# Kernel tuning notes

Measured on AMD Instinct MI355X. Metric: run time of the kernel, lower is better.

The kernel has to match this reference:

```python
import jax, jax.numpy as jnp
import numpy as np

IN_FEATURES = 2048
OUT_FEATURES = 4096
NUM_SHIFTS = 10  # perms


def setup_inputs() -> dict:
    key = jax.random.key(0)
    kx, kw = jax.random.split(key)
    x = jax.random.normal(kx, (4, 2048, IN_FEATURES), dtype=jnp.float32)
    # nn.Linear weight: (out_features, in_features), Kaiming-uniform-ish init
    bound = 1.0 / np.sqrt(IN_FEATURES)
    W = jax.random.uniform(kw, (OUT_FEATURES, IN_FEATURES), dtype=jnp.float32,
                           minval=-bound, maxval=bound)
    return {"x": x, "W": W}


def _combined_weight(W):
    # Wt: (in, out). Sum of all weight variants; sum_i(x @ W_i) == x @ sum_i(W_i).
    Wt = W.T
    Weff = Wt + jnp.flip(Wt, axis=0) + jnp.flip(Wt, axis=1)
    for i in range(NUM_SHIFTS // 2):
        Weff = Weff + jnp.roll(Wt, shift=i + 1, axis=1)
        Weff = Weff + jnp.roll(Wt, shift=i + 1, axis=0)
    return Weff  # (in, out)


def reference(x, W):
    # reg_out (x @ W.T) + flipped + rolled variants, collapsed into one GEMM
    Weff = _combined_weight(W)
    return jnp.einsum('bsi,io->bso', x, Weff)
```

## Files before the change

kernel.cpp:

```cpp
#include <hip/hip_runtime.h>
#include <hip/hip_bf16.h>
#include <stdint.h>

#define M_DIM 8192
#define K_DIM 2048
#define N_DIM 4096
#define BM 256
#define BN 256
#define BK 64
#define NT (K_DIM / BK)
#define NITER (NT / 2)

typedef __attribute__((ext_vector_type(8))) short bf16x8;
typedef __attribute__((ext_vector_type(4))) float f32x4;

__device__ __forceinline__ unsigned short f2bfu(float f) {
    __hip_bfloat16 h = __float2bfloat16(f);
    return __builtin_bit_cast(unsigned short, h);
}

__global__ __launch_bounds__(256) void prep_fused(const float* __restrict__ x,
                                                  const float* __restrict__ W,
                                                  unsigned short* __restrict__ xb,
                                                  unsigned short* __restrict__ wt) {
    const int bid = blockIdx.x;
    if (bid < N_DIM / 2) {
        __shared__ float row0[K_DIM];
        __shared__ float row1[K_DIM];
        const int o0 = bid * 2;
        const float* w0 = W + (size_t)o0 * K_DIM;
        const float* w1 = W + (size_t)(o0 + 1) * K_DIM;
#pragma unroll
        for (int t = 0; t < 2; ++t) {
            ((float4*)row0)[threadIdx.x + 256 * t] = ((const float4*)w0)[threadIdx.x + 256 * t];
            ((float4*)row1)[threadIdx.x + 256 * t] = ((const float4*)w1)[threadIdx.x + 256 * t];
        }
        __syncthreads();

        const float* rF0 = W + (size_t)(N_DIM - 1 - o0) * K_DIM;
        const float* rF1 = W + (size_t)(N_DIM - 2 - o0) * K_DIM;
        const float* rm1 = W + (size_t)((o0 - 1) & (N_DIM - 1)) * K_DIM;
        const float* rm2 = W + (size_t)((o0 - 2) & (N_DIM - 1)) * K_DIM;
        const float* rm3 = W + (size_t)((o0 - 3) & (N_DIM - 1)) * K_DIM;
        const float* rm4 = W + (size_t)((o0 - 4) & (N_DIM - 1)) * K_DIM;
        const float* rm5 = W + (size_t)((o0 - 5) & (N_DIM - 1)) * K_DIM;
        unsigned short* wo0 = wt + (size_t)o0 * K_DIM;
        unsigned short* wo1 = wo0 + K_DIM;

#pragma unroll
        for (int t = 0; t < 2; ++t) {
            const int i0 = (threadIdx.x + 256 * t) * 4;
            const float4 vF0 = *(const float4*)(rF0 + i0);
            const float4 vF1 = *(const float4*)(rF1 + i0);
            const float4 v1  = *(const float4*)(rm1 + i0);
            const float4 v2  = *(const float4*)(rm2 + i0);
            const float4 v3  = *(const float4*)(rm3 + i0);
            const float4 v4  = *(const float4*)(rm4 + i0);
            const float4 v5  = *(const float4*)(rm5 + i0);
            ushort4 ov0, ov1;
#pragma unroll
            for (int j = 0; j < 4; ++j) {
                const int i = i0 + j;
                float s0 = row0[i] + row0[K_DIM - 1 - i]
                         + row0[(i - 1) & (K_DIM - 1)] + row0[(i - 2) & (K_DIM - 1)]
                         + row0[(i - 3) & (K_DIM - 1)] + row0[(i - 4) & (K_DIM - 1)]
                         + row0[(i - 5) & (K_DIM - 1)];
                s0 += (&vF0.x)[j] + (&v1.x)[j] + (&v2.x)[j]
                    + (&v3.x)[j] + (&v4.x)[j] + (&v5.x)[j];
                (&ov0.x)[j] = f2bfu(s0);

                float s1 = row1[i] + row1[K_DIM - 1 - i]
                         + row1[(i - 1) & (K_DIM - 1)] + row1[(i - 2) & (K_DIM - 1)]
                         + row1[(i - 3) & (K_DIM - 1)] + row1[(i - 4) & (K_DIM - 1)]
                         + row1[(i - 5) & (K_DIM - 1)];
                s1 += (&vF1.x)[j] + row0[i] + (&v1.x)[j] + (&v2.x)[j]
                    + (&v3.x)[j] + (&v4.x)[j];
                (&ov1.x)[j] = f2bfu(s1);
            }
            *(ushort4*)(wo0 + i0) = ov0;
            *(ushort4*)(wo1 + i0) = ov1;
        }
    } else {
        const int idx = (bid - N_DIM / 2) * 256 + threadIdx.x;
        float4 v = ((const float4*)x)[idx];
        ushort4 o;
        o.x = f2bfu(v.x); o.y = f2bfu(v.y); o.z = f2bfu(v.z); o.w = f2bfu(v.w);
        ((ushort4*)xb)[idx] = o;
    }
}

__global__ __launch_bounds__(512, 2) void gemm8p(const unsigned short* __restrict__ Ab,
                                                 const unsigned short* __restrict__ Bt,
                                                 float* __restrict__ C) {
    __shared__ __align__(16) char smem[2 * 65536];

    const int tid  = threadIdx.x;
    const int wave = tid >> 6;
    const int lane = tid & 63;

    const int nwg = gridDim.x;
    const int cpx = nwg >> 3;
    const int wg  = (blockIdx.x & 7) * cpx + (blockIdx.x >> 3);
    const int nbn = N_DIM / BN;
    const int bm0 = (wg / nbn) * BM;
    const int bn0 = (wg % nbn) * BN;

    const int wr = wave >> 2;
    const int wc = wave & 3;

    const int srow = tid >> 3;
    const int lsw  = (lane & 7) ^ ((lane >> 3) & 7);
    const unsigned short* gA0 = Ab + (size_t)(bm0 + srow) * K_DIM + lsw * 8;
    const unsigned short* gB0 = Bt + (size_t)(bn0 + srow) * K_DIM + lsw * 8;

    const int r16  = lane & 15;
    const int x7   = lane & 7;
    const int ksl0 = (((lane >> 4)    ) ^ x7) * 16;
    const int ksl1 = (((lane >> 4) | 4) ^ x7) * 16;
    const int aRow = (wr * 128 + r16) * 128;
    const int bRow = (wc * 64  + r16) * 128 + 32768;

    f32x4  acc[8][4] = {};
    bf16x8 b[4][2];

#define STAGE_HALF(gbase, opoff, h, t, p) do {                                              \
    char* lds_ = smem + (p) * 65536 + (opoff) + (h) * 16384 + wave * 1024;                  \
    const unsigned short* g_ = (gbase) + (size_t)((h) * 128) * K_DIM + (t) * BK;            \
    __builtin_amdgcn_global_load_lds(                                                        \
        (const __attribute__((address_space(1))) unsigned int*)g_,                           \
        (__attribute__((address_space(3))) unsigned int*)lds_, 16, 0, 0);                    \
    __builtin_amdgcn_global_load_lds(                                                        \
        (const __attribute__((address_space(1))) unsigned int*)(g_ + (size_t)64 * K_DIM),    \
        (__attribute__((address_space(3))) unsigned int*)(lds_ + 8192), 16, 0, 0);           \
} while (0)

#define PHASE(P, Q, LOADB, STAGE_STMT, VM_STMT) do {                                        \
    const char* base_ = smem + (P) * 65536;                                                 \
    bf16x8 a_[2][2];                                                                        \
    if (LOADB) {                                                                            \
        _Pragma("unroll")                                                                   \
        for (int fn = 0; fn < 4; ++fn) {                                                    \
            b[fn][0] = *(const bf16x8*)(base_ + bRow + fn * 2048 + ksl0);                   \
            b[fn][1] = *(const bf16x8*)(base_ + bRow + fn * 2048 + ksl1);                   \
        }                                                                                   \
    }                                                                                       \
    a_[0][0] = *(const bf16x8*)(base_ + aRow + (Q) * 4096 + ksl0);                          \
    a_[0][1] = *(const bf16x8*)(base_ + aRow + (Q) * 4096 + ksl1);                          \
    a_[1][0] = *(const bf16x8*)(base_ + aRow + (Q) * 4096 + 2048 + ksl0);                   \
    a_[1][1] = *(const bf16x8*)(base_ + aRow + (Q) * 4096 + 2048 + ksl1);                   \
    STAGE_STMT;                                                                             \
    __builtin_amdgcn_s_barrier();                                                           \
    asm volatile("s_waitcnt lgkmcnt(0)" ::: "memory");                                      \
    __builtin_amdgcn_sched_barrier(0);                                                      \
    __builtin_amdgcn_s_setprio(1);                                                          \
    _Pragma("unroll")                                                                       \
    for (int fm = 0; fm < 2; ++fm)                                                          \
        _Pragma("unroll")                                                                   \
        for (int fn = 0; fn < 4; ++fn) {                                                    \
            acc[(Q)*2 + fm][fn] = __builtin_amdgcn_mfma_f32_16x16x32_bf16(                  \
                a_[fm][0], b[fn][0], acc[(Q)*2 + fm][fn], 0, 0, 0);                         \
            acc[(Q)*2 + fm][fn] = __builtin_amdgcn_mfma_f32_16x16x32_bf16(                  \
                a_[fm][1], b[fn][1], acc[(Q)*2 + fm][fn], 0, 0, 0);                         \
        }                                                                                   \
    __builtin_amdgcn_s_setprio(0);                                                          \
    VM_STMT;                                                                                \
    __builtin_amdgcn_s_barrier();                                                           \
} while (0)

    STAGE_HALF(gB0, 32768, 0, 0, 0);
    STAGE_HALF(gB0, 32768, 1, 0, 0);
    STAGE_HALF(gA0, 0,     0, 0, 0);
    STAGE_HALF(gA0, 0,     1, 0, 0);
    STAGE_HALF(gB0, 32768, 0, 1, 1);
    STAGE_HALF(gB0, 32768, 1, 1, 1);
    STAGE_HALF(gA0, 0,     0, 1, 1);
    asm volatile("s_waitcnt vmcnt(6)" ::: "memory");
    __builtin_amdgcn_s_barrier();

    for (int u = 0; u < NITER; ++u) {
        const bool last = (u == NITER - 1);
        const int  t1 = 2 * u + 1, t2 = 2 * u + 2, t3 = 2 * u + 3;

        PHASE(0, 0, 1, { STAGE_HALF(gA0, 0, 1, t1, 1); }, {});
        PHASE(0, 1, 0, { if (!last) STAGE_HALF(gB0, 32768, 0, t2, 0); }, {});
        PHASE(0, 2, 0, { if (!last) STAGE_HALF(gB0, 32768, 1, t2, 0); }, {});
        PHASE(0, 3, 0, { if (!last) STAGE_HALF(gA0, 0, 0, t2, 0); },
              { if (last) asm volatile("s_waitcnt vmcnt(0)" ::: "memory");
                else      asm volatile("s_waitcnt vmcnt(6)" ::: "memory"); });
        PHASE(1, 0, 1, { if (!last) STAGE_HALF(gA0, 0, 1, t2, 0); }, {});
        PHASE(1, 1, 0, { if (!last) STAGE_HALF(gB0, 32768, 0, t3, 1); }, {});
        PHASE(1, 2, 0, { if (!last) STAGE_HALF(gB0, 32768, 1, t3, 1); }, {});
        PHASE(1, 3, 0, { if (!last) STAGE_HALF(gA0, 0, 0, t3, 1); },
              { if (!last) asm volatile("s_waitcnt vmcnt(6)" ::: "memory"); });
    }
#undef PHASE
#undef STAGE_HALF

    const int crow = (lane >> 4) * 4;
    const int ccol = lane & 15;
    float* Cb = C + (size_t)(bm0 + wr * 128 + crow) * N_DIM + (bn0 + wc * 64 + ccol);
#pragma unroll
    for (int fm = 0; fm < 8; ++fm)
#pragma unroll
        for (int fn = 0; fn < 4; ++fn)
#pragma unroll
            for (int r = 0; r < 4; ++r)
                Cb[(size_t)(fm * 16 + r) * N_DIM + fn * 16] = acc[fm][fn][r];
}

extern "C" void kernel_launch(void* const* d_in, const int* in_sizes, int n_in,
                              void* d_out, int out_size, void* d_ws, size_t ws_size,
                              hipStream_t stream) {
    const float* x = (const float*)d_in[0];
    const float* W = (const float*)d_in[1];
    float* out = (float*)d_out;

    unsigned short* xb = (unsigned short*)d_ws;
    unsigned short* wt = (unsigned short*)((char*)d_ws + (size_t)M_DIM * K_DIM * 2);

    const int cvt_blocks = (M_DIM * K_DIM) / 4 / 256;
    prep_fused<<<N_DIM / 2 + cvt_blocks, 256, 0, stream>>>(x, W, xb, wt);

    dim3 grid((M_DIM / BM) * (N_DIM / BN));
    gemm8p<<<grid, 512, 0, stream>>>(xb, wt, out);
}
```

Before: 163.6 us.

## Make GEMM persistent with two tiles per workgroup and overlap epilogue with next prologue

The GEMM grid drops from 512 to 256 workgroups. Each workgroup now computes two output tiles, at M offsets 0 and 4096. The second tile's prologue global loads are issued before the first tile's C stores, so the epilogue overlaps with prefetch. The B-fragment LDS reads in the first phase are also split with staged lgkmcnt waits, letting MFMAs start before all B reads land. The cost is a fixed 256-block grid that matches the CU count, which removes tail flexibility, and the prologue writing LDS while prior reads may still be pending relies on the existing barriers.

```diff
diff --git a/kernel.cpp b/kernel.cpp
--- a/kernel.cpp
+++ b/kernel.cpp
@@ -98,20 +98,14 @@
     const int wave = tid >> 6;
     const int lane = tid & 63;
 
-    const int nwg = gridDim.x;
-    const int cpx = nwg >> 3;
-    const int wg  = (blockIdx.x & 7) * cpx + (blockIdx.x >> 3);
-    const int nbn = N_DIM / BN;
-    const int bm0 = (wg / nbn) * BM;
-    const int bn0 = (wg % nbn) * BN;
+    const int cpx = 256 >> 3;
+    const int wg  = ((int)blockIdx.x & 7) * cpx + ((int)blockIdx.x >> 3);
 
     const int wr = wave >> 2;
     const int wc = wave & 3;
 
     const int srow = tid >> 3;
     const int lsw  = (lane & 7) ^ ((lane >> 3) & 7);
-    const unsigned short* gA0 = Ab + (size_t)(bm0 + srow) * K_DIM + lsw * 8;
-    const unsigned short* gB0 = Bt + (size_t)(bn0 + srow) * K_DIM + lsw * 8;
 
     const int r16  = lane & 15;
     const int x7   = lane & 7;
@@ -119,9 +113,13 @@
     const int ksl1 = (((lane >> 4) | 4) ^ x7) * 16;
     const int aRow = (wr * 128 + r16) * 128;
     const int bRow = (wc * 64  + r16) * 128 + 32768;
-
-    f32x4  acc[8][4] = {};
+    const int crow = (lane >> 4) * 4;
+    const int ccol = lane & 15;
+
+    f32x4  acc[8][4];
     bf16x8 b[4][2];
+    const unsigned short* gA0;
+    const unsigned short* gB0;
 
 #define STAGE_HALF(gbase, opoff, h, t, p) do {                                              \
     char* lds_ = smem + (p) * 65536 + (opoff) + (h) * 16384 + wave * 1024;                  \
@@ -134,16 +132,9 @@
         (__attribute__((address_space(3))) unsigned int*)(lds_ + 8192), 16, 0, 0);           \
 } while (0)
 
-#define PHASE(P, Q, LOADB, STAGE_STMT, VM_STMT) do {                                        \
+#define PHASE(P, Q, STAGE_STMT, VM_STMT) do {                                               \
     const char* base_ = smem + (P) * 65536;                                                 \
     bf16x8 a_[2][2];                                                                        \
-    if (LOADB) {                                                                            \
-        _Pragma("unroll")                                                                   \
-        for (int fn = 0; fn < 4; ++fn) {                                                    \
-            b[fn][0] = *(const bf16x8*)(base_ + bRow + fn * 2048 + ksl0);                   \
-            b[fn][1] = *(const bf16x8*)(base_ + bRow + fn * 2048 + ksl1);                   \
-        }                                                                                   \
-    }                                                                                       \
     a_[0][0] = *(const bf16x8*)(base_ + aRow + (Q) * 4096 + ksl0);                          \
     a_[0][1] = *(const bf16x8*)(base_ + aRow + (Q) * 4096 + ksl1);                          \
     a_[1][0] = *(const bf16x8*)(base_ + aRow + (Q) * 4096 + 2048 + ksl0);                   \
@@ -167,45 +158,134 @@
     __builtin_amdgcn_s_barrier();                                                           \
 } while (0)
 
-    STAGE_HALF(gB0, 32768, 0, 0, 0);
-    STAGE_HALF(gB0, 32768, 1, 0, 0);
-    STAGE_HALF(gA0, 0,     0, 0, 0);
-    STAGE_HALF(gA0, 0,     1, 0, 0);
-    STAGE_HALF(gB0, 32768, 0, 1, 1);
-    STAGE_HALF(gB0, 32768, 1, 1, 1);
-    STAGE_HALF(gA0, 0,     0, 1, 1);
-    asm volatile("s_waitcnt vmcnt(6)" ::: "memory");
-    __builtin_amdgcn_s_barrier();
-
-    for (int u = 0; u < NITER; ++u) {
-        const bool last = (u == NITER - 1);
-        const int  t1 = 2 * u + 1, t2 = 2 * u + 2, t3 = 2 * u + 3;
-
-        PHASE(0, 0, 1, { STAGE_HALF(gA0, 0, 1, t1, 1); }, {});
-        PHASE(0, 1, 0, { if (!last) STAGE_HALF(gB0, 32768, 0, t2, 0); }, {});
-        PHASE(0, 2, 0, { if (!last) STAGE_HALF(gB0, 32768, 1, t2, 0); }, {});
-        PHASE(0, 3, 0, { if (!last) STAGE_HALF(gA0, 0, 0, t2, 0); },
-              { if (last) asm volatile("s_waitcnt vmcnt(0)" ::: "memory");
-                else      asm volatile("s_waitcnt vmcnt(6)" ::: "memory"); });
-        PHASE(1, 0, 1, { if (!last) STAGE_HALF(gA0, 0, 1, t2, 0); }, {});
-        PHASE(1, 1, 0, { if (!last) STAGE_HALF(gB0, 32768, 0, t3, 1); }, {});
-        PHASE(1, 2, 0, { if (!last) STAGE_HALF(gB0, 32768, 1, t3, 1); }, {});
-        PHASE(1, 3, 0, { if (!last) STAGE_HALF(gA0, 0, 0, t3, 1); },
-              { if (!last) asm volatile("s_waitcnt vmcnt(6)" ::: "memory"); });
-    }
+#define FN_CLUSTER(Q, FN) do {                                                              \
+    _Pragma("unroll")                                                                       \
+    for (int fm = 0; fm < 2; ++fm) {                                                        \
+        acc[(Q)*2 + fm][FN] = __builtin_amdgcn_mfma_f32_16x16x32_bf16(                      \
+            a_[fm][0], b[FN][0], acc[(Q)*2 + fm][FN], 0, 0, 0);                             \
+        acc[(Q)*2 + fm][FN] = __builtin_amdgcn_mfma_f32_16x16x32_bf16(                      \
+            a_[fm][1], b[FN][1], acc[(Q)*2 + fm][FN], 0, 0, 0);                             \
+    }                                                                                       \
+} while (0)
+
+#define PHASE_B(P, Q, STAGE_STMT, VM_STMT) do {                                             \
+    const char* base_ = smem + (P) * 65536;                                                 \
+    bf16x8 a_[2][2];                                                                        \
+    a_[0][0] = *(const bf16x8*)(base_ + aRow + (Q) * 4096 + ksl0);                          \
+    a_[0][1] = *(const bf16x8*)(base_ + aRow + (Q) * 4096 + ksl1);                          \
+    a_[1][0] = *(const bf16x8*)(base_ + aRow + (Q) * 4096 + 2048 + ksl0);                   \
+    a_[1][1] = *(const bf16x8*)(base_ + aRow + (Q) * 4096 + 2048 + ksl1);                   \
+    b[0][0] = *(const bf16x8*)(base_ + bRow + ksl0);                                        \
+    b[0][1] = *(const bf16x8*)(base_ + bRow + ksl1);                                        \
+    __builtin_amdgcn_sched_barrier(0);                                                      \
+    b[1][0] = *(const bf16x8*)(base_ + bRow + 2048 + ksl0);                                 \
+    b[1][1] = *(const bf16x8*)(base_ + bRow + 2048 + ksl1);                                 \
+    __builtin_amdgcn_sched_barrier(0);                                                      \
+    b[2][0] = *(const bf16x8*)(base_ + bRow + 4096 + ksl0);                                 \
+    b[2][1] = *(const bf16x8*)(base_ + bRow + 4096 + ksl1);                                 \
+    __builtin_amdgcn_sched_barrier(0);                                                      \
+    b[3][0] = *(const bf16x8*)(base_ + bRow + 6144 + ksl0);                                 \
+    b[3][1] = *(const bf16x8*)(base_ + bRow + 6144 + ksl1);                                 \
+    __builtin_amdgcn_sched_barrier(0);                                                      \
+    STAGE_STMT;                                                                             \
+    __builtin_amdgcn_s_barrier();                                                           \
+    asm volatile("s_waitcnt lgkmcnt(6)" ::: "memory");                                      \
+    __builtin_amdgcn_sched_barrier(0);                                                      \
+    __builtin_amdgcn_s_setprio(1);                                                          \
+    FN_CLUSTER(Q, 0);                                                                       \
+    __builtin_amdgcn_sched_barrier(0);                                                      \
+    asm volatile("s_waitcnt lgkmcnt(4)" ::: "memory");                                      \
+    __builtin_amdgcn_sched_barrier(0);                                                      \
+    FN_CLUSTER(Q, 1);                                                                       \
+    __builtin_amdgcn_sched_barrier(0);                                                      \
+    asm volatile("s_waitcnt lgkmcnt(2)" ::: "memory");                                      \
+    __builtin_amdgcn_sched_barrier(0);                                                      \
+    FN_CLUSTER(Q, 2);                                                                       \
+    __builtin_amdgcn_sched_barrier(0);                                                      \
+    asm volatile("s_waitcnt lgkmcnt(0)" ::: "memory");                                      \
+    __builtin_amdgcn_sched_barrier(0);                                                      \
+    FN_CLUSTER(Q, 3);                                                                       \
+    __builtin_amdgcn_s_setprio(0);                                                          \
+    VM_STMT;                                                                                \
+    __builtin_amdgcn_s_barrier();                                                           \
+} while (0)
+
+#define PROLOGUE() do {                                                                     \
+    STAGE_HALF(gB0, 32768, 0, 0, 0);                                                        \
+    STAGE_HALF(gB0, 32768, 1, 0, 0);                                                        \
+    STAGE_HALF(gA0, 0,     0, 0, 0);                                                        \
+    STAGE_HALF(gA0, 0,     1, 0, 0);                                                        \
+    STAGE_HALF(gB0, 32768, 0, 1, 1);                                                        \
+    STAGE_HALF(gB0, 32768, 1, 1, 1);                                                        \
+    STAGE_HALF(gA0, 0,     0, 1, 1);                                                        \
+    asm volatile("s_waitcnt vmcnt(6)" ::: "memory");                                        \
+    __builtin_amdgcn_s_barrier();                                                           \
+} while (0)
+
+#define KLOOP() do {                                                                        \
+    for (int u = 0; u < NITER; ++u) {                                                       \
+        const bool last = (u == NITER - 1);                                                 \
+        const int  t1 = 2 * u + 1, t2 = 2 * u + 2, t3 = 2 * u + 3;                          \
+        PHASE_B(0, 0, { STAGE_HALF(gA0, 0, 1, t1, 1); }, {});                               \
+        PHASE(0, 1, { if (!last) STAGE_HALF(gB0, 32768, 0, t2, 0); }, {});                  \
+        PHASE(0, 2, { if (!last) STAGE_HALF(gB0, 32768, 1, t2, 0); }, {});                  \
+        PHASE(0, 3, { if (!last) STAGE_HALF(gA0, 0, 0, t2, 0); },                           \
+              { if (last) asm volatile("s_waitcnt vmcnt(0)" ::: "memory");                  \
+                else      asm volatile("s_waitcnt vmcnt(6)" ::: "memory"); });              \
+        PHASE_B(1, 0, { if (!last) STAGE_HALF(gA0, 0, 1, t2, 0); }, {});                    \
+        PHASE(1, 1, { if (!last) STAGE_HALF(gB0, 32768, 0, t3, 1); }, {});                  \
+        PHASE(1, 2, { if (!last) STAGE_HALF(gB0, 32768, 1, t3, 1); }, {});                  \
+        PHASE(1, 3, { if (!last) STAGE_HALF(gA0, 0, 0, t3, 1); },                           \
+              { if (!last) asm volatile("s_waitcnt vmcnt(6)" ::: "memory"); });             \
+    }                                                                                       \
+} while (0)
+
+#define CSTORE(Cb) do {                                                                     \
+    _Pragma("unroll")                                                                       \
+    for (int fm = 0; fm < 8; ++fm)                                                          \
+        _Pragma("unroll")                                                                   \
+        for (int fn = 0; fn < 4; ++fn)                                                      \
+            _Pragma("unroll")                                                               \
+            for (int r = 0; r < 4; ++r)                                                     \
+                (Cb)[(size_t)(fm * 16 + r) * N_DIM + fn * 16] = acc[fm][fn][r];             \
+} while (0)
+
+#define ZERO_ACC() do {                                                                     \
+    _Pragma("unroll")                                                                       \
+    for (int i_ = 0; i_ < 8; ++i_)                                                          \
+        _Pragma("unroll")                                                                   \
+        for (int j_ = 0; j_ < 4; ++j_)                                                      \
+            acc[i_][j_] = (f32x4){0.f, 0.f, 0.f, 0.f};                                      \
+} while (0)
+
+    int bm0 = (wg >> 4) * BM;
+    int bn0 = (wg & 15) * BN;
+    gA0 = Ab + (size_t)(bm0 + srow) * K_DIM + lsw * 8;
+    gB0 = Bt + (size_t)(bn0 + srow) * K_DIM + lsw * 8;
+    float* Cb0 = C + (size_t)(bm0 + wr * 128 + crow) * N_DIM + (bn0 + wc * 64 + ccol);
+
+    PROLOGUE();
+    ZERO_ACC();
+    KLOOP();
+
+    bm0 += 4096;
+    gA0 = Ab + (size_t)(bm0 + srow) * K_DIM + lsw * 8;
+    float* Cb1 = C + (size_t)(bm0 + wr * 128 + crow) * N_DIM + (bn0 + wc * 64 + ccol);
+
+    PROLOGUE();
+    CSTORE(Cb0);
+    ZERO_ACC();
+    KLOOP();
+    CSTORE(Cb1);
+
+#undef CSTORE
+#undef ZERO_ACC
+#undef KLOOP
+#undef PROLOGUE
+#undef PHASE_B
+#undef FN_CLUSTER
 #undef PHASE
 #undef STAGE_HALF
-
-    const int crow = (lane >> 4) * 4;
-    const int ccol = lane & 15;
-    float* Cb = C + (size_t)(bm0 + wr * 128 + crow) * N_DIM + (bn0 + wc * 64 + ccol);
-#pragma unroll
-    for (int fm = 0; fm < 8; ++fm)
-#pragma unroll
-        for (int fn = 0; fn < 4; ++fn)
-#pragma unroll
-            for (int r = 0; r < 4; ++r)
-                Cb[(size_t)(fm * 16 + r) * N_DIM + fn * 16] = acc[fm][fn][r];
 }
 
 extern "C" void kernel_launch(void* const* d_in, const int* in_sizes, int n_in,
@@ -221,6 +301,5 @@
     const int cvt_blocks = (M_DIM * K_DIM) / 4 / 256;
     prep_fused<<<N_DIM / 2 + cvt_blocks, 256, 0, stream>>>(x, W, xb, wt);
 
-    dim3 grid((M_DIM / BM) * (N_DIM / BN));
-    gemm8p<<<grid, 512, 0, stream>>>(xb, wt, out);
+    gemm8p<<<256, 512, 0, stream>>>(xb, wt, out);
 }
```

After: 164.0 us. About the same (+0.2%).
